# Kernel optimization log

Measured on AMD Instinct MI355X. Metric: run time of the kernel, lower is better.

The kernel has to match this reference:

```python
import jax, jax.numpy as jnp
import numpy as np

N_NODES = 100000
N_EDGES = 1600000
D_IN, D_HID, D_OUT = 128, 128, 64


def setup_inputs() -> dict:
    key = jax.random.key(0)
    k1, k2, k3, k4 = jax.random.split(key, 4)
    x = jax.random.normal(k1, (N_NODES, D_IN), dtype=jnp.float32)
    edge_index = jax.random.randint(k2, (2, N_EDGES), 0, N_NODES, dtype=jnp.int64)
    # Glorot-style weights, zero bias (GCNConv defaults: weight + bias)
    W1 = jax.random.normal(k3, (D_IN, D_HID), dtype=jnp.float32) * (1.0 / np.sqrt(D_IN))
    b1 = jnp.zeros((D_HID,), dtype=jnp.float32)
    W2 = jax.random.normal(k4, (D_HID, D_OUT), dtype=jnp.float32) * (1.0 / np.sqrt(D_HID))
    b2 = jnp.zeros((D_OUT,), dtype=jnp.float32)
    return {"x": x, "edge_index": edge_index, "W1": W1, "b1": b1, "W2": W2, "b2": b2}


def reference(x, edge_index, W1, b1, W2, b2):
    n = x.shape[0]
    src, dst = edge_index[0], edge_index[1]
    # GCN symmetric normalization, add_self_loops=False
    ones = jnp.ones((src.shape[0],), dtype=x.dtype)
    deg = jax.ops.segment_sum(ones, dst, num_segments=n)
    deg_inv_sqrt = jnp.where(deg > 0, jax.lax.rsqrt(jnp.maximum(deg, 1.0)), 0.0)
    norm = deg_inv_sqrt[src] * deg_inv_sqrt[dst]  # [E]

    def gcn_conv(h, W, b):
        h = h @ W                                   # [N, d_out] transform first
        msg = h[src] * norm[:, None]                # [E, d_out] gather + scale
        agg = jax.ops.segment_sum(msg, dst, num_segments=n)  # scatter-add
        return agg + b

    h = jax.nn.relu(gcn_conv(x, W1, b1))
    # dropout(p=0.6) is identity in eval mode (training=False)
    return gcn_conv(h, W2, b2)
```

## Files before the change

kernel.cpp:

```cpp
#include <hip/hip_runtime.h>

#define N_NODES 100000
#define N_EDGES 1600000
#define NBUCK 391
#define CHUNKA 4096
#define NBLKA 391

typedef __bf16 bf16x8 __attribute__((ext_vector_type(8)));
typedef float f32x4 __attribute__((ext_vector_type(4)));
typedef float f32x2 __attribute__((ext_vector_type(2)));

__device__ inline unsigned short bf1(float a) {
    unsigned u = __builtin_bit_cast(unsigned, a);
    u = (u + 0x7FFF + ((u >> 16) & 1)) >> 16;
    return (unsigned short)u;
}
__device__ inline unsigned bfpack(float a, float b) {
    unsigned ua = __builtin_bit_cast(unsigned, a);
    unsigned ub = __builtin_bit_cast(unsigned, b);
    ua = (ua + 0x7FFF + ((ua >> 16) & 1)) >> 16;
    ub = (ub + 0x7FFF + ((ub >> 16) & 1)) >> 16;
    return ua | (ub << 16);
}
__device__ inline float bflo(unsigned v) { return __builtin_bit_cast(float, v << 16); }
__device__ inline float bfhi(unsigned v) { return __builtin_bit_cast(float, v & 0xFFFF0000u); }

__global__ __launch_bounds__(256) void bhist_kernel(const int* __restrict__ ei,
                                                    int* __restrict__ bhist,
                                                    const float* __restrict__ W1,
                                                    const float* __restrict__ W2,
                                                    unsigned short* __restrict__ Wt1,
                                                    unsigned short* __restrict__ Wt2) {
    const int t = threadIdx.x;
    if (blockIdx.x >= NBLKA) {
        if (blockIdx.x == NBLKA) {
            for (int i = t; i < 128 * 128; i += 256) {
                int k = i >> 7, n = i & 127;
                Wt1[n * 128 + k] = bf1(W1[i]);
            }
        } else {
            for (int i = t; i < 128 * 64; i += 256) {
                int k = i >> 6, n = i & 63;
                Wt2[n * 128 + k] = bf1(W2[i]);
            }
        }
        return;
    }
    __shared__ int hist[NBUCK];
    const int e0 = blockIdx.x * CHUNKA;
    const int n  = min(CHUNKA, N_EDGES - e0);
    for (int i = t; i < NBUCK; i += 256) hist[i] = 0;
    __syncthreads();
    const int4* __restrict__ dst4 = (const int4*)(ei + N_EDGES + e0);
    const int n4 = n >> 2;
    for (int i = t; i < n4; i += 256) {
        int4 d = dst4[i];
        atomicAdd(&hist[d.x >> 8], 1);
        atomicAdd(&hist[d.y >> 8], 1);
        atomicAdd(&hist[d.z >> 8], 1);
        atomicAdd(&hist[d.w >> 8], 1);
    }
    __syncthreads();
    for (int i = t; i < NBUCK; i += 256)
        if (hist[i]) atomicAdd(&bhist[i], hist[i]);
}

__global__ __launch_bounds__(512) void prep_kernel(const int* __restrict__ bhist,
                                                   int* __restrict__ boffs) {
    const int t = threadIdx.x;
    __shared__ int s[512];
    int v = (t < NBUCK) ? bhist[t] : 0;
    s[t] = v;
    __syncthreads();
#pragma unroll
    for (int off = 1; off < 512; off <<= 1) {
        int tv = (t >= off) ? s[t - off] : 0;
        __syncthreads();
        s[t] += tv;
        __syncthreads();
    }
    if (t < NBUCK) boffs[t] = s[t] - v;
    if (t == NBUCK - 1) boffs[NBUCK] = s[t];
}

__global__ __launch_bounds__(256) void binA_kernel(const int* __restrict__ ei,
                                                   const int* __restrict__ boffs,
                                                   int* __restrict__ bcur,
                                                   unsigned* __restrict__ epk) {
    __shared__ int hist[NBUCK], base[NBUCK], cur[NBUCK];
    const int t = threadIdx.x;
    const int e0 = blockIdx.x * CHUNKA;
    const int n  = min(CHUNKA, N_EDGES - e0);
    const int n4 = n >> 2;
    const int4* __restrict__ src4 = (const int4*)(ei + e0);
    const int4* __restrict__ dst4 = (const int4*)(ei + N_EDGES + e0);
    for (int i = t; i < NBUCK; i += 256) hist[i] = 0;
    __syncthreads();
    for (int i = t; i < n4; i += 256) {
        int4 d = dst4[i];
        atomicAdd(&hist[d.x >> 8], 1);
        atomicAdd(&hist[d.y >> 8], 1);
        atomicAdd(&hist[d.z >> 8], 1);
        atomicAdd(&hist[d.w >> 8], 1);
    }
    __syncthreads();
    for (int i = t; i < NBUCK; i += 256) {
        int h = hist[i];
        base[i] = boffs[i] + (h ? atomicAdd(&bcur[i], h) : 0);
        cur[i]  = 0;
    }
    __syncthreads();
    for (int i = t; i < n4; i += 256) {
        int4 s = src4[i];
        int4 d = dst4[i];
#define PUT(ss, dd)                                               \
        do {                                                      \
            int b = (dd) >> 8;                                    \
            int r = atomicAdd(&cur[b], 1);                        \
            epk[base[b] + r] = ((unsigned)(ss) << 8) | (unsigned)((dd) & 255); \
        } while (0)
        PUT(s.x, d.x); PUT(s.y, d.y); PUT(s.z, d.z); PUT(s.w, d.w);
#undef PUT
    }
}

__global__ __launch_bounds__(256) void binB_kernel(const unsigned* __restrict__ epk,
                                                   const int* __restrict__ boffs,
                                                   int* __restrict__ deg,
                                                   float* __restrict__ dis,
                                                   int* __restrict__ offs,
                                                   int* __restrict__ srcn) {
    __shared__ int cnt[256], s[256], loff[256];
    const int b  = blockIdx.x;
    const int t  = threadIdx.x;
    const int n0 = b << 8;
    const int base = boffs[b];
    const int end  = boffs[b + 1];
    cnt[t] = 0;
    __syncthreads();
    for (int e = base + t; e < end; e += 256)
        atomicAdd(&cnt[epk[e] & 255u], 1);
    __syncthreads();
    int v = cnt[t];
    s[t] = v;
    __syncthreads();
#pragma unroll
    for (int off = 1; off < 256; off <<= 1) {
        int tv = (t >= off) ? s[t - off] : 0;
        __syncthreads();
        s[t] += tv;
        __syncthreads();
    }
    loff[t] = s[t] - v;
    {
        int node = n0 + t;
        if (node < N_NODES) {
            deg[node]  = v;
            dis[node]  = (v > 0) ? rsqrtf((float)v) : 0.0f;
            offs[node] = base + loff[t];
        }
    }
    cnt[t] = 0;
    __syncthreads();
    for (int e = base + t; e < end; e += 256) {
        unsigned p = epk[e];
        int li  = (int)(p & 255u);
        int r   = atomicAdd(&cnt[li], 1);
        srcn[base + loff[li] + r] = (int)(p >> 8);
    }
}

__global__ __launch_bounds__(256) void gemm1_kernel(const float* __restrict__ x,
                                                    const unsigned short* __restrict__ Wt1,
                                                    const float* __restrict__ dis,
                                                    unsigned short* __restrict__ h1b) {
    __shared__ unsigned short Asm[64][136];
    __shared__ float diss[64];
    const int t = threadIdx.x;
    const int node0 = blockIdx.x * 64;

#pragma unroll
    for (int c = 0; c < 4; ++c) {
        int i = c * 256 + t;
        int row = i >> 4, ko = (i & 15) * 8;
        int gn = node0 + row;
        float4 v0 = make_float4(0, 0, 0, 0), v1 = v0;
        if (gn < N_NODES) {
            const float* p = x + (size_t)gn * 128 + ko;
            v0 = *(const float4*)p;
            v1 = *(const float4*)(p + 4);
        }
        uint4 o;
        o.x = bfpack(v0.x, v0.y); o.y = bfpack(v0.z, v0.w);
        o.z = bfpack(v1.x, v1.y); o.w = bfpack(v1.z, v1.w);
        *(uint4*)&Asm[row][ko] = o;
    }
    if (t < 64) {
        int gn = node0 + t;
        diss[t] = (gn < N_NODES) ? dis[gn] : 0.0f;
    }
    __syncthreads();

    const int wv = t >> 6, ln = t & 63;
    const int lc = ln & 15, q = ln >> 4;
    const int n0 = wv * 32;

    bf16x8 bfr[2][4];
#pragma unroll
    for (int nt = 0; nt < 2; ++nt)
#pragma unroll
        for (int k = 0; k < 4; ++k)
            bfr[nt][k] = *(const bf16x8*)(Wt1 + (size_t)(n0 + nt * 16 + lc) * 128 + k * 32 + q * 8);

    f32x4 acc[4][2];
#pragma unroll
    for (int m = 0; m < 4; ++m)
#pragma unroll
        for (int nt = 0; nt < 2; ++nt) acc[m][nt] = (f32x4)(0.0f);

#pragma unroll
    for (int k = 0; k < 4; ++k) {
        bf16x8 af[4];
#pragma unroll
        for (int m = 0; m < 4; ++m)
            af[m] = *(const bf16x8*)&Asm[m * 16 + lc][k * 32 + q * 8];
#pragma unroll
        for (int m = 0; m < 4; ++m)
#pragma unroll
            for (int nt = 0; nt < 2; ++nt)
                acc[m][nt] = __builtin_amdgcn_mfma_f32_16x16x32_bf16(af[m], bfr[nt][k], acc[m][nt], 0, 0, 0);
    }

#pragma unroll
    for (int m = 0; m < 4; ++m)
#pragma unroll
        for (int r = 0; r < 4; ++r) {
            int lr = m * 16 + q * 4 + r;
            int gn = node0 + lr;
            if (gn < N_NODES) {
                float dv = diss[lr];
#pragma unroll
                for (int nt = 0; nt < 2; ++nt)
                    h1b[(size_t)gn * 128 + n0 + nt * 16 + lc] = bf1(acc[m][nt][r] * dv);
            }
        }
}

__global__ __launch_bounds__(256) void agg1gemm2_kernel(const int* __restrict__ srcn,
                                                        const int* __restrict__ offs,
                                                        const int* __restrict__ deg,
                                                        const float* __restrict__ dis,
                                                        const unsigned short* __restrict__ h1b,
                                                        const float* __restrict__ b1,
                                                        const unsigned short* __restrict__ Wt2,
                                                        unsigned short* __restrict__ h2b) {
    __shared__ unsigned short Zs[64][136];
    __shared__ float diss[64];
    __shared__ int offs_s[64], deg_s[64];
    const int t = threadIdx.x;
    const int node0 = blockIdx.x * 64;
    if (t < 64) {
        int gn = node0 + t;
        bool ok = gn < N_NODES;
        offs_s[t] = ok ? offs[gn] : 0;
        deg_s[t]  = ok ? deg[gn] : 0;
        diss[t]   = ok ? dis[gn] : 0.0f;
    }
    __syncthreads();

    const int wv = t >> 6, ln = t & 63;
    const int qw = ln >> 4, lc = ln & 15;
    const uint4* __restrict__ h1q = (const uint4*)h1b;

    float4 bbA = *(const float4*)(b1 + lc * 8);
    float4 bbB = *(const float4*)(b1 + lc * 8 + 4);

#define ACC8(v)                                           \
    do {                                                  \
        g0 += (f32x2){bflo((v).x), bfhi((v).x)};          \
        g1 += (f32x2){bflo((v).y), bfhi((v).y)};          \
        g2 += (f32x2){bflo((v).z), bfhi((v).z)};          \
        g3 += (f32x2){bflo((v).w), bfhi((v).w)};          \
    } while (0)

    for (int r = 0; r < 4; ++r) {
        const int lr  = wv * 16 + r * 4 + qw;
        const int beg = offs_s[lr];
        const int d   = deg_s[lr];
        f32x2 g0 = (f32x2)(0.0f), g1 = (f32x2)(0.0f),
              g2 = (f32x2)(0.0f), g3 = (f32x2)(0.0f);
        int k = 0;
        for (; k + 8 <= d; k += 8) {
            int s0 = srcn[beg + k];
            int s1 = srcn[beg + k + 1];
            int s2 = srcn[beg + k + 2];
            int s3 = srcn[beg + k + 3];
            int s4 = srcn[beg + k + 4];
            int s5 = srcn[beg + k + 5];
            int s6 = srcn[beg + k + 6];
            int s7 = srcn[beg + k + 7];
            uint4 v0 = h1q[(size_t)s0 * 16 + lc];
            uint4 v1 = h1q[(size_t)s1 * 16 + lc];
            uint4 v2 = h1q[(size_t)s2 * 16 + lc];
            uint4 v3 = h1q[(size_t)s3 * 16 + lc];
            uint4 v4 = h1q[(size_t)s4 * 16 + lc];
            uint4 v5 = h1q[(size_t)s5 * 16 + lc];
            uint4 v6 = h1q[(size_t)s6 * 16 + lc];
            uint4 v7 = h1q[(size_t)s7 * 16 + lc];
            ACC8(v0); ACC8(v1); ACC8(v2); ACC8(v3);
            ACC8(v4); ACC8(v5); ACC8(v6); ACC8(v7);
        }
        for (; k + 4 <= d; k += 4) {
            int s0 = srcn[beg + k];
            int s1 = srcn[beg + k + 1];
            int s2 = srcn[beg + k + 2];
            int s3 = srcn[beg + k + 3];
            uint4 v0 = h1q[(size_t)s0 * 16 + lc];
            uint4 v1 = h1q[(size_t)s1 * 16 + lc];
            uint4 v2 = h1q[(size_t)s2 * 16 + lc];
            uint4 v3 = h1q[(size_t)s3 * 16 + lc];
            ACC8(v0); ACC8(v1); ACC8(v2); ACC8(v3);
        }
        for (; k < d; ++k) {
            int s = srcn[beg + k];
            uint4 v = h1q[(size_t)s * 16 + lc];
            ACC8(v);
        }
        float dv = diss[lr];
        uint4 o;
        o.x = bfpack(fmaxf(dv * g0.x + bbA.x, 0.0f), fmaxf(dv * g0.y + bbA.y, 0.0f));
        o.y = bfpack(fmaxf(dv * g1.x + bbA.z, 0.0f), fmaxf(dv * g1.y + bbA.w, 0.0f));
        o.z = bfpack(fmaxf(dv * g2.x + bbB.x, 0.0f), fmaxf(dv * g2.y + bbB.y, 0.0f));
        o.w = bfpack(fmaxf(dv * g3.x + bbB.z, 0.0f), fmaxf(dv * g3.y + bbB.w, 0.0f));
        *(uint4*)&Zs[lr][lc * 8] = o;
    }
#undef ACC8
    __syncthreads();

    const int lc2 = ln & 15, q = ln >> 4;
    const int n0 = wv * 16;

    bf16x8 bfr[4];
#pragma unroll
    for (int k = 0; k < 4; ++k)
        bfr[k] = *(const bf16x8*)(Wt2 + (size_t)(n0 + lc2) * 128 + k * 32 + q * 8);

    f32x4 acc[4];
#pragma unroll
    for (int m = 0; m < 4; ++m) acc[m] = (f32x4)(0.0f);

#pragma unroll
    for (int k = 0; k < 4; ++k) {
        bf16x8 af[4];
#pragma unroll
        for (int m = 0; m < 4; ++m)
            af[m] = *(const bf16x8*)&Zs[m * 16 + lc2][k * 32 + q * 8];
#pragma unroll
        for (int m = 0; m < 4; ++m)
            acc[m] = __builtin_amdgcn_mfma_f32_16x16x32_bf16(af[m], bfr[k], acc[m], 0, 0, 0);
    }

#pragma unroll
    for (int m = 0; m < 4; ++m)
#pragma unroll
        for (int r = 0; r < 4; ++r) {
            int lr = m * 16 + q * 4 + r;
            int gn = node0 + lr;
            if (gn < N_NODES) {
                float dv = diss[lr];
                h2b[(size_t)gn * 64 + n0 + lc2] = bf1(acc[m][r] * dv);
            }
        }
}

__global__ __launch_bounds__(256) void agg2_kernel(const int* __restrict__ srcn,
                                                   const int* __restrict__ offs,
                                                   const int* __restrict__ deg,
                                                   const float* __restrict__ dis,
                                                   const unsigned short* __restrict__ h2b,
                                                   const float* __restrict__ b2,
                                                   float* __restrict__ out) {
    __shared__ float diss[64];
    __shared__ int offs_s[64], deg_s[64];
    const int t = threadIdx.x;
    const int node0 = blockIdx.x * 64;
    if (t < 64) {
        int gn = node0 + t;
        bool ok = gn < N_NODES;
        offs_s[t] = ok ? offs[gn] : 0;
        deg_s[t]  = ok ? deg[gn] : 0;
        diss[t]   = ok ? dis[gn] : 0.0f;
    }
    __syncthreads();

    const int wv = t >> 6, ln = t & 63;
    const int qw = ln >> 4, lc = ln & 15;
    const uint2* __restrict__ h2v = (const uint2*)h2b;

    float4 bb = *(const float4*)(b2 + lc * 4);

#define ACC4(v)                                           \
    do {                                                  \
        g0 += (f32x2){bflo((v).x), bfhi((v).x)};          \
        g1 += (f32x2){bflo((v).y), bfhi((v).y)};          \
    } while (0)

    for (int r = 0; r < 4; ++r) {
        const int lr  = wv * 16 + r * 4 + qw;
        const int beg = offs_s[lr];
        const int d   = deg_s[lr];
        f32x2 g0 = (f32x2)(0.0f), g1 = (f32x2)(0.0f);
        int k = 0;
        for (; k + 8 <= d; k += 8) {
            int s0 = srcn[beg + k];
            int s1 = srcn[beg + k + 1];
            int s2 = srcn[beg + k + 2];
            int s3 = srcn[beg + k + 3];
            int s4 = srcn[beg + k + 4];
            int s5 = srcn[beg + k + 5];
            int s6 = srcn[beg + k + 6];
            int s7 = srcn[beg + k + 7];
            uint2 v0 = h2v[(size_t)s0 * 16 + lc];
            uint2 v1 = h2v[(size_t)s1 * 16 + lc];
            uint2 v2 = h2v[(size_t)s2 * 16 + lc];
            uint2 v3 = h2v[(size_t)s3 * 16 + lc];
            uint2 v4 = h2v[(size_t)s4 * 16 + lc];
            uint2 v5 = h2v[(size_t)s5 * 16 + lc];
            uint2 v6 = h2v[(size_t)s6 * 16 + lc];
            uint2 v7 = h2v[(size_t)s7 * 16 + lc];
            ACC4(v0); ACC4(v1); ACC4(v2); ACC4(v3);
            ACC4(v4); ACC4(v5); ACC4(v6); ACC4(v7);
        }
        for (; k + 4 <= d; k += 4) {
            int s0 = srcn[beg + k];
            int s1 = srcn[beg + k + 1];
            int s2 = srcn[beg + k + 2];
            int s3 = srcn[beg + k + 3];
            uint2 v0 = h2v[(size_t)s0 * 16 + lc];
            uint2 v1 = h2v[(size_t)s1 * 16 + lc];
            uint2 v2 = h2v[(size_t)s2 * 16 + lc];
            uint2 v3 = h2v[(size_t)s3 * 16 + lc];
            ACC4(v0); ACC4(v1); ACC4(v2); ACC4(v3);
        }
        for (; k < d; ++k) {
            int s = srcn[beg + k];
            uint2 v = h2v[(size_t)s * 16 + lc];
            ACC4(v);
        }
        int gn = node0 + lr;
        if (gn < N_NODES) {
            float dv = diss[lr];
            float4 o;
            o.x = dv * g0.x + bb.x;
            o.y = dv * g0.y + bb.y;
            o.z = dv * g1.x + bb.z;
            o.w = dv * g1.y + bb.w;
            *(float4*)(out + (size_t)gn * 64 + lc * 4) = o;
        }
    }
#undef ACC4
}

extern "C" void kernel_launch(void* const* d_in, const int* in_sizes, int n_in,
                              void* d_out, int out_size, void* d_ws, size_t ws_size,
                              hipStream_t stream) {
    const float* x  = (const float*)d_in[0];
    const int*   ei = (const int*)d_in[1];
    const float* W1 = (const float*)d_in[2];
    const float* b1 = (const float*)d_in[3];
    const float* W2 = (const float*)d_in[4];
    const float* b2 = (const float*)d_in[5];
    float* out = (float*)d_out;

    char* ws = (char*)d_ws;
    int*   bhist = (int*)(ws);
    int*   bcur  = (int*)(ws + (size_t)4 * 1024);
    int*   boffs = (int*)(ws + (size_t)8 * 1024);
    int*   deg   = (int*)(ws + (size_t)16 * 1024);
    int*   offs  = (int*)(ws + (size_t)512 * 1024);
    float* dis   = (float*)(ws + (size_t)1024 * 1024);
    unsigned short* Wt1 = (unsigned short*)(ws + (size_t)1536 * 1024);
    unsigned short* Wt2 = (unsigned short*)(ws + (size_t)1600 * 1024);
    unsigned* epk = (unsigned*)(ws + (size_t)2560 * 1024);
    int*   srcn  = (int*)(ws + (size_t)9216 * 1024);
    unsigned short* h1b = (unsigned short*)(ws + (size_t)16 * 1024 * 1024);
    unsigned short* h2b = (unsigned short*)(ws + (size_t)48 * 1024 * 1024);

    hipMemsetAsync(ws, 0, (size_t)8 * 1024, stream);

    bhist_kernel<<<NBLKA + 2, 256, 0, stream>>>(ei, bhist, W1, W2, Wt1, Wt2);
    prep_kernel<<<1, 512, 0, stream>>>(bhist, boffs);
    binA_kernel<<<NBLKA, 256, 0, stream>>>(ei, boffs, bcur, epk);
    binB_kernel<<<NBUCK, 256, 0, stream>>>(epk, boffs, deg, dis, offs, srcn);
    gemm1_kernel<<<(N_NODES + 63) / 64, 256, 0, stream>>>(x, Wt1, dis, h1b);
    agg1gemm2_kernel<<<(N_NODES + 63) / 64, 256, 0, stream>>>(srcn, offs, deg, dis,
                                                              h1b, b1, Wt2, h2b);
    agg2_kernel<<<(N_NODES + 63) / 64, 256, 0, stream>>>(srcn, offs, deg, dis,
                                                         h2b, b2, out);
}
```

Baseline: 270.8 us.

## Bin edges into fixed-stride buckets to drop the separate histogram pass

```diff
diff --git a/kernel.cpp b/kernel.cpp
--- a/kernel.cpp
+++ b/kernel.cpp
@@ -5,6 +5,7 @@
 #define NBUCK 391
 #define CHUNKA 4096
 #define NBLKA 391
+#define ESTRIDE 6144
 
 typedef __bf16 bf16x8 __attribute__((ext_vector_type(8)));
 typedef float f32x4 __attribute__((ext_vector_type(4)));
@@ -25,12 +26,13 @@
 __device__ inline float bflo(unsigned v) { return __builtin_bit_cast(float, v << 16); }
 __device__ inline float bfhi(unsigned v) { return __builtin_bit_cast(float, v & 0xFFFF0000u); }
 
-__global__ __launch_bounds__(256) void bhist_kernel(const int* __restrict__ ei,
-                                                    int* __restrict__ bhist,
-                                                    const float* __restrict__ W1,
-                                                    const float* __restrict__ W2,
-                                                    unsigned short* __restrict__ Wt1,
-                                                    unsigned short* __restrict__ Wt2) {
+__global__ __launch_bounds__(256) void binA_kernel(const int* __restrict__ ei,
+                                                   int* __restrict__ bcur,
+                                                   unsigned* __restrict__ epk,
+                                                   const float* __restrict__ W1,
+                                                   const float* __restrict__ W2,
+                                                   unsigned short* __restrict__ Wt1,
+                                                   unsigned short* __restrict__ Wt2) {
     const int t = threadIdx.x;
     if (blockIdx.x >= NBLKA) {
         if (blockIdx.x == NBLKA) {
@@ -46,13 +48,14 @@
         }
         return;
     }
-    __shared__ int hist[NBUCK];
+    __shared__ int hist[NBUCK], base[NBUCK], cur[NBUCK];
     const int e0 = blockIdx.x * CHUNKA;
     const int n  = min(CHUNKA, N_EDGES - e0);
+    const int n4 = n >> 2;
+    const int4* __restrict__ src4 = (const int4*)(ei + e0);
+    const int4* __restrict__ dst4 = (const int4*)(ei + N_EDGES + e0);
     for (int i = t; i < NBUCK; i += 256) hist[i] = 0;
     __syncthreads();
-    const int4* __restrict__ dst4 = (const int4*)(ei + N_EDGES + e0);
-    const int n4 = n >> 2;
     for (int i = t; i < n4; i += 256) {
         int4 d = dst4[i];
         atomicAdd(&hist[d.x >> 8], 1);
@@ -61,52 +64,9 @@
         atomicAdd(&hist[d.w >> 8], 1);
     }
     __syncthreads();
-    for (int i = t; i < NBUCK; i += 256)
-        if (hist[i]) atomicAdd(&bhist[i], hist[i]);
-}
-
-__global__ __launch_bounds__(512) void prep_kernel(const int* __restrict__ bhist,
-                                                   int* __restrict__ boffs) {
-    const int t = threadIdx.x;
-    __shared__ int s[512];
-    int v = (t < NBUCK) ? bhist[t] : 0;
-    s[t] = v;
-    __syncthreads();
-#pragma unroll
-    for (int off = 1; off < 512; off <<= 1) {
-        int tv = (t >= off) ? s[t - off] : 0;
-        __syncthreads();
-        s[t] += tv;
-        __syncthreads();
-    }
-    if (t < NBUCK) boffs[t] = s[t] - v;
-    if (t == NBUCK - 1) boffs[NBUCK] = s[t];
-}
-
-__global__ __launch_bounds__(256) void binA_kernel(const int* __restrict__ ei,
-                                                   const int* __restrict__ boffs,
-                                                   int* __restrict__ bcur,
-                                                   unsigned* __restrict__ epk) {
-    __shared__ int hist[NBUCK], base[NBUCK], cur[NBUCK];
-    const int t = threadIdx.x;
-    const int e0 = blockIdx.x * CHUNKA;
-    const int n  = min(CHUNKA, N_EDGES - e0);
-    const int n4 = n >> 2;
-    const int4* __restrict__ src4 = (const int4*)(ei + e0);
-    const int4* __restrict__ dst4 = (const int4*)(ei + N_EDGES + e0);
-    for (int i = t; i < NBUCK; i += 256) hist[i] = 0;
-    __syncthreads();
-    for (int i = t; i < n4; i += 256) {
-        int4 d = dst4[i];
-        atomicAdd(&hist[d.x >> 8], 1);
-        atomicAdd(&hist[d.y >> 8], 1);
-        atomicAdd(&hist[d.z >> 8], 1);
-        atomicAdd(&hist[d.w >> 8], 1);
-    }
-    __syncthreads();
     for (int i = t; i < NBUCK; i += 256) {
         int h = hist[i];
-        base[i] = boffs[i] + (h ? atomicAdd(&bcur[i], h) : 0);
+        base[i] = i * ESTRIDE + (h ? atomicAdd(&bcur[i], h) : 0);
         cur[i]  = 0;
     }
     __syncthreads();
@@ -124,7 +84,26 @@
     }
 }
 
+__global__ __launch_bounds__(512) void prep_kernel(const int* __restrict__ bcur,
+                                                   int* __restrict__ boffs) {
+    const int t = threadIdx.x;
+    __shared__ int s[512];
+    int v = (t < NBUCK) ? bcur[t] : 0;
+    s[t] = v;
+    __syncthreads();
+#pragma unroll
+    for (int off = 1; off < 512; off <<= 1) {
+        int tv = (t >= off) ? s[t - off] : 0;
+        __syncthreads();
+        s[t] += tv;
+        __syncthreads();
+    }
+    if (t < NBUCK) boffs[t] = s[t] - v;
+    if (t == NBUCK - 1) boffs[NBUCK] = s[t];
+}
+
 __global__ __launch_bounds__(256) void binB_kernel(const unsigned* __restrict__ epk,
+                                                   const int* __restrict__ bcur,
                                                    const int* __restrict__ boffs,
                                                    int* __restrict__ deg,
                                                    float* __restrict__ dis,
@@ -134,8 +113,9 @@
     const int b  = blockIdx.x;
     const int t  = threadIdx.x;
     const int n0 = b << 8;
-    const int base = boffs[b];
-    const int end  = boffs[b + 1];
+    const int base  = b * ESTRIDE;
+    const int end   = base + bcur[b];
+    const int sbase = boffs[b];
     cnt[t] = 0;
     __syncthreads();
     for (int e = base + t; e < end; e += 256)
@@ -157,7 +137,7 @@
         if (node < N_NODES) {
             deg[node]  = v;
             dis[node]  = (v > 0) ? rsqrtf((float)v) : 0.0f;
-            offs[node] = base + loff[t];
+            offs[node] = sbase + loff[t];
         }
     }
     cnt[t] = 0;
@@ -166,7 +146,7 @@
         unsigned p = epk[e];
         int li  = (int)(p & 255u);
         int r   = atomicAdd(&cnt[li], 1);
-        srcn[base + loff[li] + r] = (int)(p >> 8);
+        srcn[sbase + loff[li] + r] = (int)(p >> 8);
     }
 }
 
@@ -473,25 +453,23 @@
     float* out = (float*)d_out;
 
     char* ws = (char*)d_ws;
-    int*   bhist = (int*)(ws);
-    int*   bcur  = (int*)(ws + (size_t)4 * 1024);
-    int*   boffs = (int*)(ws + (size_t)8 * 1024);
+    int*   bcur  = (int*)(ws);
+    int*   boffs = (int*)(ws + (size_t)4 * 1024);
     int*   deg   = (int*)(ws + (size_t)16 * 1024);
     int*   offs  = (int*)(ws + (size_t)512 * 1024);
     float* dis   = (float*)(ws + (size_t)1024 * 1024);
     unsigned short* Wt1 = (unsigned short*)(ws + (size_t)1536 * 1024);
     unsigned short* Wt2 = (unsigned short*)(ws + (size_t)1600 * 1024);
     unsigned* epk = (unsigned*)(ws + (size_t)2560 * 1024);
-    int*   srcn  = (int*)(ws + (size_t)9216 * 1024);
-    unsigned short* h1b = (unsigned short*)(ws + (size_t)16 * 1024 * 1024);
-    unsigned short* h2b = (unsigned short*)(ws + (size_t)48 * 1024 * 1024);
-
-    hipMemsetAsync(ws, 0, (size_t)8 * 1024, stream);
-
-    bhist_kernel<<<NBLKA + 2, 256, 0, stream>>>(ei, bhist, W1, W2, Wt1, Wt2);
-    prep_kernel<<<1, 512, 0, stream>>>(bhist, boffs);
-    binA_kernel<<<NBLKA, 256, 0, stream>>>(ei, boffs, bcur, epk);
-    binB_kernel<<<NBUCK, 256, 0, stream>>>(epk, boffs, deg, dis, offs, srcn);
+    int*   srcn  = (int*)(ws + (size_t)12800 * 1024);
+    unsigned short* h1b = (unsigned short*)(ws + (size_t)20 * 1024 * 1024);
+    unsigned short* h2b = (unsigned short*)(ws + (size_t)46 * 1024 * 1024);
+
+    hipMemsetAsync(ws, 0, (size_t)2 * 1024, stream);
+
+    binA_kernel<<<NBLKA + 2, 256, 0, stream>>>(ei, bcur, epk, W1, W2, Wt1, Wt2);
+    prep_kernel<<<1, 512, 0, stream>>>(bcur, boffs);
+    binB_kernel<<<NBUCK, 256, 0, stream>>>(epk, bcur, boffs, deg, dis, offs, srcn);
     gemm1_kernel<<<(N_NODES + 63) / 64, 256, 0, stream>>>(x, Wt1, dis, h1b);
     agg1gemm2_kernel<<<(N_NODES + 63) / 64, 256, 0, stream>>>(srcn, offs, deg, dis,
                                                               h1b, b1, Wt2, h2b);
```

Measured after the change: 257.1 us. 5.1% less time.
